# Optimization experiments

Measured on AMD Instinct MI355X. Metric: run time of the kernel, lower is better.

The kernel has to match this reference:

```python
import jax, jax.numpy as jnp
import numpy as np

H = 128  # hidden_size

def setup_inputs() -> dict:
    key = jax.random.key(0)
    ks = jax.random.split(key, 12)
    B, SEQ = 256, 1000
    static = jax.random.normal(ks[0], (B, 2, SEQ), jnp.float32)
    dynamic = jax.random.uniform(ks[1], (B, 2, SEQ), jnp.float32)
    # Encoder = 1x1 Conv1d(in_ch -> H): weight (H, in_ch), bias (H,)
    def xavier(k, shape):
        fan_in, fan_out = shape[1], shape[0]
        lim = np.sqrt(6.0 / (fan_in + fan_out)).astype(np.float32)
        return jax.random.uniform(k, shape, jnp.float32, -lim, lim)
    enc_s_w = xavier(ks[2], (H, 2)); enc_s_b = jnp.zeros((H,), jnp.float32)
    enc_d_w = xavier(ks[3], (H, 2)); enc_d_b = jnp.zeros((H,), jnp.float32)
    v = xavier(ks[4], (1, H))[0]                 # attention vector (H,)
    W = xavier(ks[5], (H, 3 * H))                # attention matrix (H, 3H)
    dense_w = xavier(ks[6], (H, 128)); dense_b = jnp.zeros((H,), jnp.float32)
    lin_w = xavier(ks[7], (1, H)); lin_b = jnp.zeros((1,), jnp.float32)
    return {"static": static, "dynamic": dynamic,
            "enc_s_w": enc_s_w, "enc_s_b": enc_s_b,
            "enc_d_w": enc_d_w, "enc_d_b": enc_d_b,
            "v": v, "W": W,
            "dense_w": dense_w, "dense_b": dense_b,
            "lin_w": lin_w, "lin_b": lin_b}


def reference(static, dynamic, enc_s_w, enc_s_b, enc_d_w, enc_d_b,
              v, W, dense_w, dense_b, lin_w, lin_b):
    B = static.shape[0]
    # 1x1-conv encoders (computed once; identical across loop iterations)
    e = jnp.einsum('hc,bcs->bhs', enc_s_w, static) + enc_s_b[None, :, None]   # (B,H,S)
    dyn_ld = jnp.broadcast_to(dynamic[:, 1:2, :], dynamic.shape)              # load channel expanded
    d = jnp.einsum('hc,bcs->bhs', enc_d_w, dyn_ld) + enc_d_b[None, :, None]   # (B,H,S)
    hy = jnp.zeros((B, H), static.dtype)
    for _ in range(3):  # fixed 3-step refinement loop
        hidden = jnp.concatenate(
            [e, d, jnp.broadcast_to(hy[:, :, None], e.shape)], axis=1)        # (B,3H,S)
        u = jnp.tanh(jnp.einsum('hk,bks->bhs', W, hidden))                    # (B,H,S)
        logit = jnp.einsum('h,bhs->bs', v, u)                                 # (B,S)
        prob = jax.nn.softmax(logit, axis=-1)
        hy = jnp.einsum('bs,bhs->bh', prob, e)                                # context update
    out = jax.nn.relu(hy @ dense_w.T + dense_b) @ lin_w.T + lin_b             # (B,1)
    return out
```

## Files before the change

kernel.cpp:

```cpp
#include <hip/hip_runtime.h>
#include <math.h>

#define HH 128
#define SS 1000
#define NT 1024
#define NW (NT / 64)

#define C1 2.8853900817779268f
#define C2 1.4426950408889634f

typedef float v2f __attribute__((ext_vector_type(2)));

template <int CTRL>
__device__ __forceinline__ float dpp_add(float x) {
    int s = __builtin_amdgcn_update_dpp(0, __builtin_bit_cast(int, x),
                                        CTRL, 0xF, 0xF, true);
    return x + __builtin_bit_cast(float, s);
}

__global__ __launch_bounds__(NT) void sc_fused(
    const float* __restrict__ stat, const float* __restrict__ dyn,
    const float* __restrict__ enc_s_w, const float* __restrict__ enc_s_b,
    const float* __restrict__ enc_d_w, const float* __restrict__ enc_d_b,
    const float* __restrict__ v, const float* __restrict__ W,
    const float* __restrict__ dense_w, const float* __restrict__ dense_b,
    const float* __restrict__ lin_w, const float* __restrict__ lin_b,
    float* __restrict__ out) {
    const int b    = blockIdx.x;
    const int t    = threadIdx.x;
    const int wave = t >> 6;
    const int lane = t & 63;
    const int g    = t & 31;
    const int sg   = t >> 5;

    __shared__ __align__(16) float4 xs[NT];
    __shared__ __align__(16) float kc[8][HH];
    __shared__ float4 red4[2][NW];
    __shared__ float hy_sh[HH];
    __shared__ float svc2_sh;

    {
        float x0 = 0.f, x1 = 0.f, yv = 0.f;
        if (t < SS) {
            const float* sb = stat + (size_t)b * 2 * SS;
            x0 = sb[t];
            x1 = sb[SS + t];
            yv = dyn[(size_t)b * 2 * SS + SS + t];
        }
        xs[t] = make_float4(x0, x1, yv, 0.f);
    }

    {
        const int fh = t >> 3;
        const int fq = t & 7;
        const float4* W1 = (const float4*)(W + fh * (3 * HH));
        const float4* W2 = (const float4*)(W + fh * (3 * HH) + HH);
        const float4* W3 = (const float4*)(W + fh * (3 * HH) + 2 * HH);
        const float4* ES = (const float4*)enc_s_w;
        const float4* ED = (const float4*)enc_d_w;
        const float4* SB = (const float4*)enc_s_b;
        const float4* DB = (const float4*)enc_d_b;
        float a0 = 0.f, a1 = 0.f, ad = 0.f, cc = 0.f, w30 = 0.f, w31 = 0.f, w3b = 0.f;
        #pragma unroll
        for (int j = 0; j < 4; ++j) {
            const int k4 = fq * 4 + j;
            float4 w1 = W1[k4], w2 = W2[k4], w3 = W3[k4];
            float4 e01 = ES[2 * k4], e23 = ES[2 * k4 + 1];
            float4 d01 = ED[2 * k4], d23 = ED[2 * k4 + 1];
            float4 sb = SB[k4], db = DB[k4];
            a0 = fmaf(w1.x, e01.x, a0); a0 = fmaf(w1.y, e01.z, a0);
            a0 = fmaf(w1.z, e23.x, a0); a0 = fmaf(w1.w, e23.z, a0);
            a1 = fmaf(w1.x, e01.y, a1); a1 = fmaf(w1.y, e01.w, a1);
            a1 = fmaf(w1.z, e23.y, a1); a1 = fmaf(w1.w, e23.w, a1);
            ad = fmaf(w2.x, d01.x + d01.y, ad); ad = fmaf(w2.y, d01.z + d01.w, ad);
            ad = fmaf(w2.z, d23.x + d23.y, ad); ad = fmaf(w2.w, d23.z + d23.w, ad);
            cc = fmaf(w1.x, sb.x, cc); cc = fmaf(w1.y, sb.y, cc);
            cc = fmaf(w1.z, sb.z, cc); cc = fmaf(w1.w, sb.w, cc);
            cc = fmaf(w2.x, db.x, cc); cc = fmaf(w2.y, db.y, cc);
            cc = fmaf(w2.z, db.z, cc); cc = fmaf(w2.w, db.w, cc);
            w30 = fmaf(w3.x, e01.x, w30); w30 = fmaf(w3.y, e01.z, w30);
            w30 = fmaf(w3.z, e23.x, w30); w30 = fmaf(w3.w, e23.z, w30);
            w31 = fmaf(w3.x, e01.y, w31); w31 = fmaf(w3.y, e01.w, w31);
            w31 = fmaf(w3.z, e23.y, w31); w31 = fmaf(w3.w, e23.w, w31);
            w3b = fmaf(w3.x, sb.x, w3b); w3b = fmaf(w3.y, sb.y, w3b);
            w3b = fmaf(w3.z, sb.z, w3b); w3b = fmaf(w3.w, sb.w, w3b);
        }
        a0  = dpp_add<0x111>(a0);  a0  = dpp_add<0x112>(a0);  a0  = dpp_add<0x114>(a0);
        a1  = dpp_add<0x111>(a1);  a1  = dpp_add<0x112>(a1);  a1  = dpp_add<0x114>(a1);
        ad  = dpp_add<0x111>(ad);  ad  = dpp_add<0x112>(ad);  ad  = dpp_add<0x114>(ad);
        cc  = dpp_add<0x111>(cc);  cc  = dpp_add<0x112>(cc);  cc  = dpp_add<0x114>(cc);
        w30 = dpp_add<0x111>(w30); w30 = dpp_add<0x112>(w30); w30 = dpp_add<0x114>(w30);
        w31 = dpp_add<0x111>(w31); w31 = dpp_add<0x112>(w31); w31 = dpp_add<0x114>(w31);
        w3b = dpp_add<0x111>(w3b); w3b = dpp_add<0x112>(w3b); w3b = dpp_add<0x114>(w3b);
        if (fq == 7) {
            kc[0][fh] = a0 * C1;
            kc[1][fh] = a1 * C1;
            kc[2][fh] = ad * C1;
            kc[4][fh] = cc * C1;
            kc[5][fh] = (cc + w3b) * C1;
            kc[6][fh] = w30 * C1;
            kc[7][fh] = w31 * C1;
        }
        if (t < HH) kc[3][t] = v[t];
        if (t < 32) {
            float4 x = ((const float4*)v)[t];
            float s = (x.x + x.y) + (x.z + x.w);
            #pragma unroll
            for (int off = 1; off < 32; off <<= 1) s += __shfl_xor(s, off);
            if (t == 0) svc2_sh = s * C2;
        }
    }
    __syncthreads();

    const int h4 = g * 4;
    float4 u;
    u = *(const float4*)&kc[0][h4]; const v2f a0_0 = {u.x, u.y}, a0_1 = {u.z, u.w};
    u = *(const float4*)&kc[1][h4]; const v2f a1_0 = {u.x, u.y}, a1_1 = {u.z, u.w};
    u = *(const float4*)&kc[2][h4]; const v2f ad_0 = {u.x, u.y}, ad_1 = {u.z, u.w};
    u = *(const float4*)&kc[3][h4]; const v2f vv_0 = {u.x, u.y}, vv_1 = {u.z, u.w};
    const float svc2 = svc2_sh;
    const v2f one2 = {1.f, 1.f};
    const bool owner = (g == 31);

    float X0 = 0.f, X1 = 0.f;

    for (int iter = 0; iter < 3; ++iter) {
        v2f cg_0, cg_1;
        if (iter == 0) {
            u = *(const float4*)&kc[4][h4];
            cg_0 = (v2f){u.x, u.y};
            cg_1 = (v2f){u.z, u.w};
        } else {
            float4 ub = *(const float4*)&kc[5][h4];
            float4 u0 = *(const float4*)&kc[6][h4];
            float4 u1 = *(const float4*)&kc[7][h4];
            v2f X0v = {X0, X0}, X1v = {X1, X1};
            cg_0 = __builtin_elementwise_fma(
                (v2f){u0.x, u0.y}, X0v,
                __builtin_elementwise_fma((v2f){u1.x, u1.y}, X1v, (v2f){ub.x, ub.y}));
            cg_1 = __builtin_elementwise_fma(
                (v2f){u0.z, u0.w}, X0v,
                __builtin_elementwise_fma((v2f){u1.z, u1.w}, X1v, (v2f){ub.z, ub.w}));
        }

        float S = 0.f, Sx0 = 0.f, Sx1 = 0.f;
        #pragma unroll 2
        for (int pass = 0; pass < 32; ++pass) {
            const int s = pass * 32 + sg;
            float4 x = xs[s];
            v2f vx0 = {x.x, x.x}, vx1 = {x.y, x.y}, vyv = {x.z, x.z};
            v2f z0 = __builtin_elementwise_fma(
                a0_0, vx0, __builtin_elementwise_fma(
                    a1_0, vx1, __builtin_elementwise_fma(ad_0, vyv, cg_0)));
            v2f z1 = __builtin_elementwise_fma(
                a0_1, vx0, __builtin_elementwise_fma(
                    a1_1, vx1, __builtin_elementwise_fma(ad_1, vyv, cg_1)));
            v2f e0, e1;
            e0.x = __builtin_amdgcn_exp2f(z0.x);
            e0.y = __builtin_amdgcn_exp2f(z0.y);
            e1.x = __builtin_amdgcn_exp2f(z1.x);
            e1.y = __builtin_amdgcn_exp2f(z1.y);
            v2f d0 = e0 + one2, d1 = e1 + one2;
            v2f r0, r1;
            r0.x = __builtin_amdgcn_rcpf(d0.x);
            r0.y = __builtin_amdgcn_rcpf(d0.y);
            r1.x = __builtin_amdgcn_rcpf(d1.x);
            r1.y = __builtin_amdgcn_rcpf(d1.y);
            v2f acc2 = __builtin_elementwise_fma(vv_0, r0, (v2f){0.f, 0.f});
            acc2 = __builtin_elementwise_fma(vv_1, r1, acc2);
            float acc = acc2.x + acc2.y;
            acc = dpp_add<0x111>(acc);
            acc = dpp_add<0x112>(acc);
            acc = dpp_add<0x114>(acc);
            acc = dpp_add<0x118>(acc);
            acc = dpp_add<0x142>(acc);
            const bool own = owner && (s < SS);
            float arg = own ? fmaf(-C1, acc, svc2) : -200.f;
            float p = __builtin_amdgcn_exp2f(arg);
            S   += p;
            Sx0  = fmaf(p, x.x, Sx0);
            Sx1  = fmaf(p, x.y, Sx1);
        }
        S   += __shfl_xor(S, 32);
        Sx0 += __shfl_xor(Sx0, 32);
        Sx1 += __shfl_xor(Sx1, 32);
        if (lane == 31) red4[iter & 1][wave] = make_float4(S, Sx0, Sx1, 0.f);
        __syncthreads();
        float4 w4 = red4[iter & 1][lane & 15];
        #pragma unroll
        for (int off = 1; off < 16; off <<= 1) {
            w4.x += __shfl_xor(w4.x, off);
            w4.y += __shfl_xor(w4.y, off);
            w4.z += __shfl_xor(w4.z, off);
        }
        float inv = __builtin_amdgcn_rcpf(w4.x);
        X0 = w4.y * inv;
        X1 = w4.z * inv;
    }

    if (t < HH)
        hy_sh[t] = fmaf(enc_s_w[2 * t], X0, fmaf(enc_s_w[2 * t + 1], X1, enc_s_b[t]));
    __syncthreads();

    float o = 0.f;
    if (t < HH) {
        const float4* dw4 = (const float4*)(dense_w + t * HH);
        const float4* hy4 = (const float4*)hy_sh;
        float r = dense_b[t];
        #pragma unroll 4
        for (int k = 0; k < HH / 4; ++k) {
            float4 d4 = dw4[k], h4v = hy4[k];
            r = fmaf(d4.x, h4v.x, fmaf(d4.y, h4v.y, fmaf(d4.z, h4v.z, fmaf(d4.w, h4v.w, r))));
        }
        o = lin_w[t] * fmaxf(r, 0.f);
    }
    #pragma unroll
    for (int off = 32; off > 0; off >>= 1) o += __shfl_xor(o, off);
    if (lane == 0) red4[0][wave].x = o;
    __syncthreads();
    if (t == 0) {
        float s = 0.f;
        for (int i = 0; i < NW; ++i) s += red4[0][i].x;
        out[b] = s + lin_b[0];
    }
}

extern "C" void kernel_launch(void* const* d_in, const int* in_sizes, int n_in,
                              void* d_out, int out_size, void* d_ws, size_t ws_size,
                              hipStream_t stream) {
    const float* stat    = (const float*)d_in[0];
    const float* dyn     = (const float*)d_in[1];
    const float* enc_s_w = (const float*)d_in[2];
    const float* enc_s_b = (const float*)d_in[3];
    const float* enc_d_w = (const float*)d_in[4];
    const float* enc_d_b = (const float*)d_in[5];
    const float* v       = (const float*)d_in[6];
    const float* W       = (const float*)d_in[7];
    const float* dense_w = (const float*)d_in[8];
    const float* dense_b = (const float*)d_in[9];
    const float* lin_w   = (const float*)d_in[10];
    const float* lin_b   = (const float*)d_in[11];
    float* out = (float*)d_out;

    const int B = in_sizes[0] / (2 * SS);

    hipLaunchKernelGGL(sc_fused, dim3(B), dim3(NT), 0, stream,
                       stat, dyn, enc_s_w, enc_s_b, enc_d_w, enc_d_b, v, W,
                       dense_w, dense_b, lin_w, lin_b, out);
}
```

Before: 50.30 us.

## Merge sigmoid reciprocals algebraically and defer softmax exponent to a parallel pass

Each thread now combines four sigmoid terms into a single fraction with one reciprocal instead of four. The exponents are clamped to keep the product of denominators finite. The per-position softmax exponent and weighted sums no longer run serially on owner lanes inside the pass loop. Logits go to shared memory and are exponentiated by all threads afterwards, with a tree reduction. The main loop unroll rises to 4. This trades some extra shared memory, another barrier per iteration and a small precision risk from the clamp for fewer transcendental ops in the hot loop.

```diff
diff --git a/kernel.cpp b/kernel.cpp
--- a/kernel.cpp
+++ b/kernel.cpp
@@ -35,19 +35,21 @@
 
     __shared__ __align__(16) float4 xs[NT];
     __shared__ __align__(16) float kc[8][HH];
-    __shared__ float4 red4[2][NW];
+    __shared__ float logit_sh[NT];
+    __shared__ float4 red4[NW];
     __shared__ float hy_sh[HH];
     __shared__ float svc2_sh;
 
+    float x0r = 0.f, x1r = 0.f;
     {
-        float x0 = 0.f, x1 = 0.f, yv = 0.f;
+        float yv = 0.f;
         if (t < SS) {
             const float* sb = stat + (size_t)b * 2 * SS;
-            x0 = sb[t];
-            x1 = sb[SS + t];
-            yv = dyn[(size_t)b * 2 * SS + SS + t];
-        }
-        xs[t] = make_float4(x0, x1, yv, 0.f);
+            x0r = sb[t];
+            x1r = sb[SS + t];
+            yv  = dyn[(size_t)b * 2 * SS + SS + t];
+        }
+        xs[t] = make_float4(x0r, x1r, yv, 0.f);
     }
 
     {
@@ -118,8 +120,10 @@
     u = *(const float4*)&kc[1][h4]; const v2f a1_0 = {u.x, u.y}, a1_1 = {u.z, u.w};
     u = *(const float4*)&kc[2][h4]; const v2f ad_0 = {u.x, u.y}, ad_1 = {u.z, u.w};
     u = *(const float4*)&kc[3][h4]; const v2f vv_0 = {u.x, u.y}, vv_1 = {u.z, u.w};
+    const float c01 = vv_0.x + vv_0.y;
+    const float c23 = vv_1.x + vv_1.y;
     const float svc2 = svc2_sh;
-    const v2f one2 = {1.f, 1.f};
+    const v2f clampv = {28.f, 28.f};
     const bool owner = (g == 31);
 
     float X0 = 0.f, X1 = 0.f;
@@ -143,8 +147,7 @@
                 __builtin_elementwise_fma((v2f){u1.z, u1.w}, X1v, (v2f){ub.z, ub.w}));
         }
 
-        float S = 0.f, Sx0 = 0.f, Sx1 = 0.f;
-        #pragma unroll 2
+        #pragma unroll 4
         for (int pass = 0; pass < 32; ++pass) {
             const int s = pass * 32 + sg;
             float4 x = xs[s];
@@ -155,38 +158,41 @@
             v2f z1 = __builtin_elementwise_fma(
                 a0_1, vx0, __builtin_elementwise_fma(
                     a1_1, vx1, __builtin_elementwise_fma(ad_1, vyv, cg_1)));
-            v2f e0, e1;
-            e0.x = __builtin_amdgcn_exp2f(z0.x);
-            e0.y = __builtin_amdgcn_exp2f(z0.y);
-            e1.x = __builtin_amdgcn_exp2f(z1.x);
-            e1.y = __builtin_amdgcn_exp2f(z1.y);
-            v2f d0 = e0 + one2, d1 = e1 + one2;
-            v2f r0, r1;
-            r0.x = __builtin_amdgcn_rcpf(d0.x);
-            r0.y = __builtin_amdgcn_rcpf(d0.y);
-            r1.x = __builtin_amdgcn_rcpf(d1.x);
-            r1.y = __builtin_amdgcn_rcpf(d1.y);
-            v2f acc2 = __builtin_elementwise_fma(vv_0, r0, (v2f){0.f, 0.f});
-            acc2 = __builtin_elementwise_fma(vv_1, r1, acc2);
-            float acc = acc2.x + acc2.y;
+            z0 = __builtin_elementwise_min(z0, clampv);
+            z1 = __builtin_elementwise_min(z1, clampv);
+            float e0 = __builtin_amdgcn_exp2f(z0.x);
+            float e1 = __builtin_amdgcn_exp2f(z0.y);
+            float e2 = __builtin_amdgcn_exp2f(z1.x);
+            float e3 = __builtin_amdgcn_exp2f(z1.y);
+            float t1  = 1.f + e1, t3 = 1.f + e3;
+            float d01 = fmaf(e0, t1, t1);
+            float d23 = fmaf(e2, t3, t3);
+            float n01 = fmaf(vv_0.x, e1, fmaf(vv_0.y, e0, c01));
+            float n23 = fmaf(vv_1.x, e3, fmaf(vv_1.y, e2, c23));
+            float num = fmaf(n01, d23, n23 * d01);
+            float den = d01 * d23;
+            float acc = num * __builtin_amdgcn_rcpf(den);
             acc = dpp_add<0x111>(acc);
             acc = dpp_add<0x112>(acc);
             acc = dpp_add<0x114>(acc);
             acc = dpp_add<0x118>(acc);
             acc = dpp_add<0x142>(acc);
-            const bool own = owner && (s < SS);
-            float arg = own ? fmaf(-C1, acc, svc2) : -200.f;
-            float p = __builtin_amdgcn_exp2f(arg);
-            S   += p;
-            Sx0  = fmaf(p, x.x, Sx0);
-            Sx1  = fmaf(p, x.y, Sx1);
-        }
-        S   += __shfl_xor(S, 32);
-        Sx0 += __shfl_xor(Sx0, 32);
-        Sx1 += __shfl_xor(Sx1, 32);
-        if (lane == 31) red4[iter & 1][wave] = make_float4(S, Sx0, Sx1, 0.f);
+            if (owner) logit_sh[s] = acc;
+        }
         __syncthreads();
-        float4 w4 = red4[iter & 1][lane & 15];
+
+        float pp = 0.f;
+        if (t < SS) pp = __builtin_amdgcn_exp2f(fmaf(-C1, logit_sh[t], svc2));
+        float S = pp, Sx0 = pp * x0r, Sx1 = pp * x1r;
+        #pragma unroll
+        for (int off = 32; off > 0; off >>= 1) {
+            S   += __shfl_xor(S, off);
+            Sx0 += __shfl_xor(Sx0, off);
+            Sx1 += __shfl_xor(Sx1, off);
+        }
+        if (lane == 0) red4[wave] = make_float4(S, Sx0, Sx1, 0.f);
+        __syncthreads();
+        float4 w4 = red4[lane & 15];
         #pragma unroll
         for (int off = 1; off < 16; off <<= 1) {
             w4.x += __shfl_xor(w4.x, off);
@@ -216,11 +222,11 @@
     }
     #pragma unroll
     for (int off = 32; off > 0; off >>= 1) o += __shfl_xor(o, off);
-    if (lane == 0) red4[0][wave].x = o;
+    if (lane == 0) red4[wave].x = o;
     __syncthreads();
     if (t == 0) {
         float s = 0.f;
-        for (int i = 0; i < NW; ++i) s += red4[0][i].x;
+        for (int i = 0; i < NW; ++i) s += red4[i].x;
         out[b] = s + lin_b[0];
     }
 }
```

Result: slower. 55.48 us (+10.3%).
